# Kernel optimization log

Measured on AMD Instinct MI355X. Metric: run time of the kernel, lower is better.

The kernel has to match this reference:

```python
import jax, jax.numpy as jnp
import numpy as np

NUM_DISPARITIES = 48
IS_RIGHT = False
CLAMP = 1000.0


def setup_inputs() -> dict:
    key = jax.random.key(0)
    k1, k2 = jax.random.split(key)
    B, C, H, W = 2, 32, 136, 240
    left = jax.random.normal(k1, (B, C, H, W), dtype=jnp.float32)
    right = jax.random.normal(k2, (B, C, H, W), dtype=jnp.float32)
    return {"left": left, "right": right}


def reference(left, right):
    # Faithful to cost_volume(left, right, NUM_DISPARITIES, IS_RIGHT) followed by
    # the float32 cast + clamp(-1000, 1000) from forward_with_amp.
    left = left.astype(jnp.float32)
    right = right.astype(jnp.float32)
    B, C, H, W = left.shape
    D = NUM_DISPARITIES
    d = jnp.arange(D)[:, None]        # (D, 1)
    w = jnp.arange(W)[None, :]        # (1, W)
    if not IS_RIGHT:
        # out[b,c,i,h,w] = left[b,c,h,w] * right[b,c,h,w-i] for w >= i else 0
        src = w - d                   # (D, W) index into right along width
        valid = src >= 0
        gathered = jnp.take(right, jnp.clip(src, 0, W - 1), axis=3)  # (B,C,H,D,W)
        gathered = jnp.moveaxis(gathered, 3, 2)                      # (B,C,D,H,W)
        out = left[:, :, None, :, :] * gathered
    else:
        # out[b,c,i,h,w] = left[b,c,h,w+i] * right[b,c,h,w] for w < W-i else 0
        src = w + d                   # (D, W) index into left along width
        valid = src <= W - 1
        gathered = jnp.take(left, jnp.clip(src, 0, W - 1), axis=3)   # (B,C,H,D,W)
        gathered = jnp.moveaxis(gathered, 3, 2)                      # (B,C,D,H,W)
        out = gathered * right[:, :, None, :, :]
    out = jnp.where(valid[None, None, :, None, :], out, jnp.float32(0.0))
    return jnp.clip(out, -CLAMP, CLAMP)
```

## Files before the change

### kernel.cpp

```cpp
#include <hip/hip_runtime.h>
#include <hip/hip_bf16.h>

constexpr int B = 2, C = 32, H = 136, W = 240, D = 48;
constexpr int W4      = W / 4;
constexpr int PLANE   = H * W;
constexpr int PLANE4  = PLANE / 4;
constexpr int NPLANES = B * C * D;
constexpr float CLAMP = 1000.0f;

typedef float v4f __attribute__((ext_vector_type(4)));

__device__ __forceinline__ float clampv(float x) {
    return fminf(CLAMP, fmaxf(-CLAMP, x));
}

__global__ __launch_bounds__(256) void CostVolume_4939212390829_kernel(
        const float* __restrict__ left,
        const float* __restrict__ right,
        float* __restrict__ out) {
    const int p  = blockIdx.x;
    const int bc = p / D;
    const int d  = p % D;

    const float* __restrict__ lplane = left  + (size_t)bc * PLANE;
    const float* __restrict__ rplane = right + (size_t)bc * PLANE;
    float* __restrict__ oplane = out + (size_t)p * PLANE;

    for (int i = threadIdx.x; i < PLANE4; i += 256) {
        const int h = i / W4;
        const int w = (i - h * W4) * 4;
        const int row = h * W;

        const v4f l4 = *(const v4f*)(lplane + row + w);

        const float* __restrict__ rrow = rplane + row + (w - d);
        float r0 = (w + 0 >= d) ? rrow[0] : 0.0f;
        float r1 = (w + 1 >= d) ? rrow[1] : 0.0f;
        float r2 = (w + 2 >= d) ? rrow[2] : 0.0f;
        float r3 = (w + 3 >= d) ? rrow[3] : 0.0f;

        v4f o4;
        o4.x = clampv(l4.x * r0);
        o4.y = clampv(l4.y * r1);
        o4.z = clampv(l4.z * r2);
        o4.w = clampv(l4.w * r3);

        __builtin_nontemporal_store(o4, (v4f*)(oplane + i * 4));
    }
}

extern "C" void kernel_launch(void* const* d_in, const int* in_sizes, int n_in,
                              void* d_out, int out_size, void* d_ws, size_t ws_size,
                              hipStream_t stream) {
    const float* left  = (const float*)d_in[0];
    const float* right = (const float*)d_in[1];
    float* out = (float*)d_out;
    (void)in_sizes; (void)n_in; (void)out_size; (void)d_ws; (void)ws_size;

    CostVolume_4939212390829_kernel<<<NPLANES, 256, 0, stream>>>(left, right, out);
}
```

Measured before the change: 496.4 us.

## Restructure cost volume to stage right rows in LDS and loop over disparities

Each block now handles one (b,c) pair and four image rows, with one wavefront per row. The right row goes into LDS with a zero-padded prefix, and each left value is held in registers while the block emits all 48 disparity planes from shifted LDS reads. This removes the repeated global loads of left and right per disparity and the per-element bounds checks. In exchange, each thread issues strided stores across planes and 4 of 64 lanes per wave sit idle, since W4 is 60.

```diff
diff --git a/kernel.cpp b/kernel.cpp
--- a/kernel.cpp
+++ b/kernel.cpp
@@ -1,51 +1,73 @@
 #include <hip/hip_runtime.h>
-#include <hip/hip_bf16.h>
 
 constexpr int B = 2, C = 32, H = 136, W = 240, D = 48;
-constexpr int W4      = W / 4;
-constexpr int PLANE   = H * W;
-constexpr int PLANE4  = PLANE / 4;
-constexpr int NPLANES = B * C * D;
-constexpr float CLAMP = 1000.0f;
+constexpr int W4     = W / 4;
+constexpr int PLANE  = H * W;
+constexpr int ROWS   = 4;
+constexpr int HCHUNK = H / ROWS;
+constexpr int NBLK   = B * C * HCHUNK;
+constexpr float CLAMPV = 1000.0f;
+
+constexpr int LROW = 312;
 
 typedef float v4f __attribute__((ext_vector_type(4)));
 
 __device__ __forceinline__ float clampv(float x) {
-    return fminf(CLAMP, fmaxf(-CLAMP, x));
+    return fminf(CLAMPV, fmaxf(-CLAMPV, x));
 }
 
 __global__ __launch_bounds__(256) void CostVolume_4939212390829_kernel(
         const float* __restrict__ left,
         const float* __restrict__ right,
         float* __restrict__ out) {
-    const int p  = blockIdx.x;
-    const int bc = p / D;
-    const int d  = p % D;
+    const int blk  = blockIdx.x;
+    const int bc   = blk / HCHUNK;
+    const int h0   = (blk - bc * HCHUNK) * ROWS;
+    const int g    = threadIdx.x >> 6;
+    const int lane = threadIdx.x & 63;
+    const int h    = h0 + g;
 
-    const float* __restrict__ lplane = left  + (size_t)bc * PLANE;
-    const float* __restrict__ rplane = right + (size_t)bc * PLANE;
-    float* __restrict__ oplane = out + (size_t)p * PLANE;
+    __shared__ v4f lds_v[ROWS * (LROW / 4)];
+    float* lrow = reinterpret_cast<float*>(lds_v) + g * LROW;
 
-    for (int i = threadIdx.x; i < PLANE4; i += 256) {
-        const int h = i / W4;
-        const int w = (i - h * W4) * 4;
-        const int row = h * W;
+    const size_t inoff = (size_t)bc * PLANE + (size_t)h * W;
 
-        const v4f l4 = *(const v4f*)(lplane + row + w);
+    if (lane < 16) {
+        v4f z = {0.0f, 0.0f, 0.0f, 0.0f};
+        *reinterpret_cast<v4f*>(lrow + 4 * lane) = z;
+    }
 
-        const float* __restrict__ rrow = rplane + row + (w - d);
-        float r0 = (w + 0 >= d) ? rrow[0] : 0.0f;
-        float r1 = (w + 1 >= d) ? rrow[1] : 0.0f;
-        float r2 = (w + 2 >= d) ? rrow[2] : 0.0f;
-        float r3 = (w + 3 >= d) ? rrow[3] : 0.0f;
+    v4f l4 = {0.0f, 0.0f, 0.0f, 0.0f};
+    if (lane < W4) {
+        *reinterpret_cast<v4f*>(lrow + 64 + 4 * lane) =
+            *reinterpret_cast<const v4f*>(right + inoff + 4 * lane);
+        l4 = *reinterpret_cast<const v4f*>(left + inoff + 4 * lane);
+    }
 
-        v4f o4;
-        o4.x = clampv(l4.x * r0);
-        o4.y = clampv(l4.y * r1);
-        o4.z = clampv(l4.z * r2);
-        o4.w = clampv(l4.w * r3);
+    if (lane >= W4) return;
 
-        __builtin_nontemporal_store(o4, (v4f*)(oplane + i * 4));
+    const float* px0 = lrow + 60 + 4 * lane;
+    const uint32_t obase = (uint32_t)(bc * D) * PLANE + (uint32_t)h * W + 4 * lane;
+
+    for (int q = 0; q < D / 4; ++q) {
+        const float* px = px0 - 4 * q;
+        const v4f X = *reinterpret_cast<const v4f*>(px);
+        const v4f Y = *reinterpret_cast<const v4f*>(px + 4);
+        const uint32_t o0 = obase + (uint32_t)(4 * q) * PLANE;
+
+        v4f o;
+        o.x = clampv(l4.x * Y.x); o.y = clampv(l4.y * Y.y);
+        o.z = clampv(l4.z * Y.z); o.w = clampv(l4.w * Y.w);
+        __builtin_nontemporal_store(o, reinterpret_cast<v4f*>(out + o0));
+        o.x = clampv(l4.x * X.w); o.y = clampv(l4.y * Y.x);
+        o.z = clampv(l4.z * Y.y); o.w = clampv(l4.w * Y.z);
+        __builtin_nontemporal_store(o, reinterpret_cast<v4f*>(out + o0 + PLANE));
+        o.x = clampv(l4.x * X.z); o.y = clampv(l4.y * X.w);
+        o.z = clampv(l4.z * Y.x); o.w = clampv(l4.w * Y.y);
+        __builtin_nontemporal_store(o, reinterpret_cast<v4f*>(out + o0 + 2 * PLANE));
+        o.x = clampv(l4.x * X.y); o.y = clampv(l4.y * X.z);
+        o.z = clampv(l4.z * X.w); o.w = clampv(l4.w * Y.x);
+        __builtin_nontemporal_store(o, reinterpret_cast<v4f*>(out + o0 + 3 * PLANE));
     }
 }
 
@@ -57,5 +79,5 @@
     float* out = (float*)d_out;
     (void)in_sizes; (void)n_in; (void)out_size; (void)d_ws; (void)ws_size;
 
-    CostVolume_4939212390829_kernel<<<NPLANES, 256, 0, stream>>>(left, right, out);
+    CostVolume_4939212390829_kernel<<<NBLK, 256, 0, stream>>>(left, right, out);
 }
```

After: 399.9 us. -19.4%, faster.

## Stage right rows in LDS and compute all disparities per block

Applied to the files above, without the earlier changes.

Each block now loads a 17-row strip of one right channel plane into shared memory with a zero-padded left margin. Each of its 8 waves then produces 6 disparities using aligned vector LDS reads, with the misalignment handled by a templated shift. This replaces one block per output plane that did unaligned scalar global loads of the right input, so it cuts redundant global reads and removes the per-element bounds checks. The kernel is still dominated by the output writes, and the grid shrinks to 512 blocks with lanes 60-63 of every wave idle.

```diff
diff --git a/kernel.cpp b/kernel.cpp
--- a/kernel.cpp
+++ b/kernel.cpp
@@ -1,51 +1,89 @@
 #include <hip/hip_runtime.h>
-#include <hip/hip_bf16.h>
 
 constexpr int B = 2, C = 32, H = 136, W = 240, D = 48;
-constexpr int W4      = W / 4;
-constexpr int PLANE   = H * W;
-constexpr int PLANE4  = PLANE / 4;
-constexpr int NPLANES = B * C * D;
-constexpr float CLAMP = 1000.0f;
+constexpr int W4     = W / 4;
+constexpr int PLANE  = H * W;
+constexpr int RROWS  = 17;
+constexpr int HCH    = H / RROWS;
+constexpr int NBLK   = B * C * HCH;
+constexpr int LDS_ROW4 = 76;
+constexpr float CLAMPV = 1000.0f;
 
 typedef float v4f __attribute__((ext_vector_type(4)));
 
 __device__ __forceinline__ float clampv(float x) {
-    return fminf(CLAMP, fmaxf(-CLAMP, x));
+    return fminf(CLAMPV, fmaxf(-CLAMPV, x));
 }
 
-__global__ __launch_bounds__(256) void CostVolume_4939212390829_kernel(
+template<int A>
+__device__ __forceinline__ void compute_wave(
+        const float* __restrict__ srow, int lane, int w, int bc, int h0,
+        const float* __restrict__ lbase, float* __restrict__ out) {
+    constexpr int M = (4 - A) & 3;
+    #pragma unroll
+    for (int k = 0; k < 6; ++k) {
+        const int d = 8 * k + w;
+        const v4f* __restrict__ px =
+            (const v4f*)srow + ((64 - d - M + 4 * lane) >> 2);
+        float* __restrict__ obase =
+            out + (size_t)(bc * D + d) * PLANE + (size_t)h0 * W + 4 * lane;
+        #pragma unroll 4
+        for (int r = 0; r < RROWS; ++r) {
+            const v4f X = px[r * LDS_ROW4];
+            v4f Y = X;
+            if constexpr (A != 0) Y = px[r * LDS_ROW4 + 1];
+            const v4f l4 = *(const v4f*)(lbase + r * W);
+            float win[4];
+            #pragma unroll
+            for (int e = 0; e < 4; ++e) {
+                const int idx = M + e;
+                win[e] = (idx < 4) ? X[idx] : Y[idx - 4];
+            }
+            v4f o;
+            o.x = clampv(l4.x * win[0]);
+            o.y = clampv(l4.y * win[1]);
+            o.z = clampv(l4.z * win[2]);
+            o.w = clampv(l4.w * win[3]);
+            __builtin_nontemporal_store(o, (v4f*)(obase + r * W));
+        }
+    }
+}
+
+__global__ __launch_bounds__(512) void CostVolume_4939212390829_kernel(
         const float* __restrict__ left,
         const float* __restrict__ right,
         float* __restrict__ out) {
-    const int p  = blockIdx.x;
-    const int bc = p / D;
-    const int d  = p % D;
+    const int blk = blockIdx.x;
+    const int bc  = blk / HCH;
+    const int h0  = (blk - bc * HCH) * RROWS;
+    const int tid = threadIdx.x;
 
-    const float* __restrict__ lplane = left  + (size_t)bc * PLANE;
-    const float* __restrict__ rplane = right + (size_t)bc * PLANE;
-    float* __restrict__ oplane = out + (size_t)p * PLANE;
+    __shared__ v4f sR[RROWS * LDS_ROW4];
 
-    for (int i = threadIdx.x; i < PLANE4; i += 256) {
-        const int h = i / W4;
-        const int w = (i - h * W4) * 4;
-        const int row = h * W;
+    for (int i = tid; i < RROWS * 16; i += 512) {
+        const int r = i >> 4, c = i & 15;
+        sR[r * LDS_ROW4 + c] = (v4f){0.f, 0.f, 0.f, 0.f};
+    }
+    const float* __restrict__ rbase = right + (size_t)bc * PLANE + (size_t)h0 * W;
+    for (int i = tid; i < RROWS * W4; i += 512) {
+        const int r = i / W4, c = i - r * W4;
+        sR[r * LDS_ROW4 + 16 + c] = *(const v4f*)(rbase + r * W + 4 * c);
+    }
+    __syncthreads();
 
-        const v4f l4 = *(const v4f*)(lplane + row + w);
+    const int w    = tid >> 6;
+    const int lane = tid & 63;
+    if (lane >= W4) return;
 
-        const float* __restrict__ rrow = rplane + row + (w - d);
-        float r0 = (w + 0 >= d) ? rrow[0] : 0.0f;
-        float r1 = (w + 1 >= d) ? rrow[1] : 0.0f;
-        float r2 = (w + 2 >= d) ? rrow[2] : 0.0f;
-        float r3 = (w + 3 >= d) ? rrow[3] : 0.0f;
+    const float* __restrict__ lbase =
+        left + (size_t)bc * PLANE + (size_t)h0 * W + 4 * lane;
+    const float* __restrict__ srow = (const float*)sR;
 
-        v4f o4;
-        o4.x = clampv(l4.x * r0);
-        o4.y = clampv(l4.y * r1);
-        o4.z = clampv(l4.z * r2);
-        o4.w = clampv(l4.w * r3);
-
-        __builtin_nontemporal_store(o4, (v4f*)(oplane + i * 4));
+    switch (w & 3) {
+        case 0: compute_wave<0>(srow, lane, w, bc, h0, lbase, out); break;
+        case 1: compute_wave<1>(srow, lane, w, bc, h0, lbase, out); break;
+        case 2: compute_wave<2>(srow, lane, w, bc, h0, lbase, out); break;
+        case 3: compute_wave<3>(srow, lane, w, bc, h0, lbase, out); break;
     }
 }
 
@@ -57,5 +95,5 @@
     float* out = (float*)d_out;
     (void)in_sizes; (void)n_in; (void)out_size; (void)d_ws; (void)ws_size;
 
-    CostVolume_4939212390829_kernel<<<NPLANES, 256, 0, stream>>>(left, right, out);
+    CostVolume_4939212390829_kernel<<<NBLK, 512, 0, stream>>>(left, right, out);
 }
```

After: 416.5 us. 1.19x faster.

## Tile by row slabs, stage right rows in LDS, compute all disparities per block

Applied to the files above, without the earlier changes.

Each block now handles an 8-row slab of one (b,c) plane and produces all 48 disparity planes for it. The right rows are staged in shared memory with zero padding, so shifted reads need no bounds checks. Left values stay in registers and are reused across 12 disparities per wavefront. This removes repeated global reads and per-element index division, at the cost of fewer blocks and ordinary rather than nontemporal stores.

```diff
diff --git a/kernel.cpp b/kernel.cpp
--- a/kernel.cpp
+++ b/kernel.cpp
@@ -1,51 +1,85 @@
 #include <hip/hip_runtime.h>
-#include <hip/hip_bf16.h>
 
 constexpr int B = 2, C = 32, H = 136, W = 240, D = 48;
-constexpr int W4      = W / 4;
-constexpr int PLANE   = H * W;
-constexpr int PLANE4  = PLANE / 4;
-constexpr int NPLANES = B * C * D;
-constexpr float CLAMP = 1000.0f;
+constexpr int PLANE  = H * W;
+constexpr int SLABR  = 8;
+constexpr int NSLAB  = H / SLABR;
+constexpr int NBLK   = B * C * NSLAB;
+constexpr int SLAB4  = SLABR * W / 4;
+constexpr int LROW4  = 76;
+constexpr float CLAMPV = 1000.0f;
 
 typedef float v4f __attribute__((ext_vector_type(4)));
 
 __device__ __forceinline__ float clampv(float x) {
-    return fminf(CLAMP, fmaxf(-CLAMP, x));
+    return fminf(CLAMPV, fmaxf(-CLAMPV, x));
 }
+__device__ __forceinline__ int div60(int s) { return (s * 2185) >> 17; }
 
 __global__ __launch_bounds__(256) void CostVolume_4939212390829_kernel(
         const float* __restrict__ left,
         const float* __restrict__ right,
         float* __restrict__ out) {
-    const int p  = blockIdx.x;
-    const int bc = p / D;
-    const int d  = p % D;
+    const int blk  = blockIdx.x;
+    const int bc   = blk / NSLAB;
+    const int h0   = (blk - bc * NSLAB) * SLABR;
+    const int tid  = threadIdx.x;
+    const int g    = tid >> 6;
+    const int lane = tid & 63;
 
-    const float* __restrict__ lplane = left  + (size_t)bc * PLANE;
-    const float* __restrict__ rplane = right + (size_t)bc * PLANE;
-    float* __restrict__ oplane = out + (size_t)p * PLANE;
+    __shared__ v4f sR[SLABR * LROW4];
 
-    for (int i = threadIdx.x; i < PLANE4; i += 256) {
-        const int h = i / W4;
-        const int w = (i - h * W4) * 4;
-        const int row = h * W;
+    const v4f* __restrict__ rbase4 =
+        (const v4f*)(right + (size_t)bc * PLANE + (size_t)h0 * W);
+    const v4f* __restrict__ lbase4 =
+        (const v4f*)(left  + (size_t)bc * PLANE + (size_t)h0 * W);
 
-        const v4f l4 = *(const v4f*)(lplane + row + w);
+    if (tid < 128) sR[(tid >> 4) * LROW4 + (tid & 15)] = (v4f){0.f,0.f,0.f,0.f};
+    for (int i = tid; i < SLAB4; i += 256) {
+        const int r = div60(i);
+        sR[i + 16 * r + 16] = rbase4[i];
+    }
+    __syncthreads();
 
-        const float* __restrict__ rrow = rplane + row + (w - d);
-        float r0 = (w + 0 >= d) ? rrow[0] : 0.0f;
-        float r1 = (w + 1 >= d) ? rrow[1] : 0.0f;
-        float r2 = (w + 2 >= d) ? rrow[2] : 0.0f;
-        float r3 = (w + 3 >= d) ? rrow[3] : 0.0f;
+    v4f      l4[8];
+    int      q0slot[8];
+    uint32_t ob[8];
+    const uint32_t oBase0 = (uint32_t)(bc * D + 12 * g) * PLANE + (uint32_t)h0 * W;
+    #pragma unroll
+    for (int c = 0; c < 8; ++c) {
+        int s  = 64 * c + lane;
+        int ss = (s < SLAB4) ? s : (SLAB4 - 1);
+        const int r = div60(ss);
+        l4[c]      = lbase4[ss];
+        q0slot[c]  = ss + 16 * r + 16 - 3 * g;
+        ob[c]      = oBase0 + 4u * (uint32_t)ss;
+    }
 
-        v4f o4;
-        o4.x = clampv(l4.x * r0);
-        o4.y = clampv(l4.y * r1);
-        o4.z = clampv(l4.z * r2);
-        o4.w = clampv(l4.w * r3);
-
-        __builtin_nontemporal_store(o4, (v4f*)(oplane + i * 4));
+    #pragma unroll
+    for (int c = 0; c < 8; ++c) {
+        const bool act = (c < 7) || (lane < 32);
+        #pragma unroll
+        for (int q = 0; q < 3; ++q) {
+            const int slot = q0slot[c] - q;
+            const v4f Q = sR[slot];
+            const v4f P = sR[slot - 1];
+            if (act) {
+                float* __restrict__ o0 = out + ob[c] + (uint32_t)(4 * q) * PLANE;
+                v4f v;
+                v.x = clampv(l4[c].x * Q.x); v.y = clampv(l4[c].y * Q.y);
+                v.z = clampv(l4[c].z * Q.z); v.w = clampv(l4[c].w * Q.w);
+                *(v4f*)(o0) = v;
+                v.x = clampv(l4[c].x * P.w); v.y = clampv(l4[c].y * Q.x);
+                v.z = clampv(l4[c].z * Q.y); v.w = clampv(l4[c].w * Q.z);
+                *(v4f*)(o0 + PLANE) = v;
+                v.x = clampv(l4[c].x * P.z); v.y = clampv(l4[c].y * P.w);
+                v.z = clampv(l4[c].z * Q.x); v.w = clampv(l4[c].w * Q.y);
+                *(v4f*)(o0 + 2 * PLANE) = v;
+                v.x = clampv(l4[c].x * P.y); v.y = clampv(l4[c].y * P.z);
+                v.z = clampv(l4[c].z * P.w); v.w = clampv(l4[c].w * Q.x);
+                *(v4f*)(o0 + 3 * PLANE) = v;
+            }
+        }
     }
 }
 
@@ -57,5 +91,5 @@
     float* out = (float*)d_out;
     (void)in_sizes; (void)n_in; (void)out_size; (void)d_ws; (void)ws_size;
 
-    CostVolume_4939212390829_kernel<<<NPLANES, 256, 0, stream>>>(left, right, out);
+    CostVolume_4939212390829_kernel<<<NBLK, 256, 0, stream>>>(left, right, out);
 }
```

After: 410.8 us. 1.21x faster.
